# Performance work log

Hardware: AMD Instinct MI355X
Metric: run time of the kernel (lower is better)

Reference implementation:

```python
import jax, jax.numpy as jnp
import numpy as np

N = 1048576          # nodes at current depth (children), divisible by 8
M = N // 8           # non-empty parent nodes (conv outputs)
NNUM_PARENT = 262144 # total parent nodes at depth-1
C_IN = 128
C_OUT = 256


def setup_inputs() -> dict:
    key = jax.random.key(0)
    k1, k2, k3 = jax.random.split(key, 3)
    data = jax.random.normal(k1, (N, C_IN), dtype=jnp.float32)
    weights = jax.random.normal(k2, (8, C_IN, C_OUT), dtype=jnp.float32) * (1.0 / np.sqrt(8 * C_IN))
    # sorted unique positions of non-empty parents within [0, NNUM_PARENT)
    perm = jax.random.permutation(k3, NNUM_PARENT)
    nempty_idx = jnp.sort(perm[:M]).astype(jnp.int32)
    return {"data": data, "weights": weights, "nempty_idx": nempty_idx,
            "nnum_parent": NNUM_PARENT}


def reference(data, weights, nempty_idx, nnum_parent):
    # kernel-2 stride-2 conv: each consecutive group of 8 children -> one parent
    c_in, c_out = weights.shape[1], weights.shape[2]
    out = data.reshape(-1, 8 * c_in) @ weights.reshape(8 * c_in, c_out)  # [M, C_out]
    # octree_pad at depth-1: scatter into all parent nodes, zeros at empty ones
    full = jnp.zeros((nnum_parent, c_out), dtype=out.dtype).at[nempty_idx].set(out)
    return full
```

## Files before the change

### kernel.cpp

```cpp
#include <hip/hip_runtime.h>
#include <hip/hip_bf16.h>

typedef float f32x4 __attribute__((ext_vector_type(4)));
typedef short s16x8 __attribute__((ext_vector_type(8)));

using bf16 = __hip_bfloat16;

namespace {
constexpr int KD = 1024;
constexpr int BM = 128;
constexpr int BK = 32;
constexpr int NT = KD / BK;
constexpr int MBLK = 131072 / BM;
constexpr int ZBLK = 512;
}

typedef __attribute__((address_space(1))) const void GVoid;
typedef __attribute__((address_space(3))) void LVoid;

__device__ __forceinline__ void gld16(const void* g, void* l) {
  __builtin_amdgcn_global_load_lds((GVoid*)g, (LVoid*)l, 16, 0, 0);
}

__device__ __forceinline__ s16x8 cvt8(f32x4 a, f32x4 b) {
  union { s16x8 v; bf16 h[8]; } u;
#pragma unroll
  for (int j = 0; j < 4; ++j) u.h[j] = __float2bfloat16(a[j]);
#pragma unroll
  for (int j = 0; j < 4; ++j) u.h[j + 4] = __float2bfloat16(b[j]);
  return u.v;
}

__global__ void k_transpose_w(const float* __restrict__ w, bf16* __restrict__ bt) {
  int t = blockIdx.x * 256 + threadIdx.x;
  int n = t & 255;
  int k0 = (t >> 8) << 3;
  union { s16x8 v; bf16 h[8]; } u;
#pragma unroll
  for (int j = 0; j < 8; ++j)
    u.h[j] = __float2bfloat16(w[(size_t)(k0 + j) * 256 + n]);
  *(s16x8*)(bt + (size_t)n * KD + k0) = u.v;
}

__global__ void k_clear_flags(int* __restrict__ flags, int np4) {
  int i = blockIdx.x * 256 + threadIdx.x;
  if (i < np4) ((int4*)flags)[i] = make_int4(0, 0, 0, 0);
}

__global__ void k_set_flags(const int* __restrict__ idx, int* __restrict__ flags, int m) {
  int i = blockIdx.x * 256 + threadIdx.x;
  if (i < m) flags[idx[i]] = 1;
}

__global__ __launch_bounds__(512, 4)
void k_fused(const float* __restrict__ A, const bf16* __restrict__ Bt,
             const int* __restrict__ idx, const int* __restrict__ flags,
             float* __restrict__ out, int NP) {
  __shared__ float As[4][BM * BK];

  const int tid = threadIdx.x;
  const int lane = tid & 63;
  const int wave = tid >> 6;
  const int bid = blockIdx.x;

  if (bid % 3 == 2) {
    const int zb = bid / 3;
    const f32x4 z = {0.f, 0.f, 0.f, 0.f};
    for (int row = zb * 8 + wave; row < NP; row += ZBLK * 8) {
      if (flags[row] == 0)
        *(f32x4*)(out + (size_t)row * 256 + lane * 4) = z;
    }
    return;
  }

  const int gid = (bid / 3) * 2 + (bid % 3);
  const int m0 = gid * BM;
  const int wm = wave >> 2;
  const int wn = wave & 3;

  const int as0 = tid, as1 = 512 + tid;
  const int ar0 = as0 >> 3, ac0 = (as0 & 7) ^ (ar0 & 6);
  const int ar1 = as1 >> 3, ac1 = (as1 & 7) ^ (ar1 & 6);
  const float* aSrc0 = A + (size_t)(m0 + ar0) * KD + ac0 * 4;
  const float* aSrc1 = A + (size_t)(m0 + ar1) * KD + ac1 * 4;
  const int aOff0 = (wave * 64) * 4;
  const int aOff1 = (512 + wave * 64) * 4;

  const int r = lane & 15;
  const int kc = lane >> 4;

  const int arow = wm * 64 + r;
  const int aRd = arow * 32 + (((2 * kc) ^ (arow & 6)) * 4);

  const bf16* bp0 = Bt + (size_t)(wn * 64 + r) * KD + kc * 8;
  const bf16* bp1 = bp0 + (size_t)16 * KD;
  const bf16* bp2 = bp0 + (size_t)32 * KD;
  const bf16* bp3 = bp0 + (size_t)48 * KD;

  f32x4 acc[4][4] = {};

  auto stage = [&](int buf, int t) {
    gld16(aSrc0 + t * BK, &As[buf][aOff0]);
    gld16(aSrc1 + t * BK, &As[buf][aOff1]);
  };

  stage(0, 0);
  stage(1, 1);
  stage(2, 2);

#pragma unroll 1
  for (int t = 0; t < NT; ++t) {
    if (t >= 2 && t < NT - 2) {
      asm volatile("s_waitcnt vmcnt(12)" ::: "memory");
    } else if (t == 1) {
      asm volatile("s_waitcnt vmcnt(8)" ::: "memory");
    } else {
      asm volatile("s_waitcnt vmcnt(4)" ::: "memory");
    }
    __builtin_amdgcn_s_barrier();

    s16x8 bfr0 = *(const s16x8*)(bp0 + t * BK);
    s16x8 bfr1 = *(const s16x8*)(bp1 + t * BK);
    s16x8 bfr2 = *(const s16x8*)(bp2 + t * BK);
    s16x8 bfr3 = *(const s16x8*)(bp3 + t * BK);
    asm volatile("" ::: "memory");

    if (t + 3 < NT) stage((t + 3) & 3, t + 3);

    const int cur = t & 3;
#pragma unroll
    for (int fm = 0; fm < 4; ++fm) {
      f32x4 lo = *(const f32x4*)(&As[cur][aRd + fm * 512]);
      f32x4 hi = *(const f32x4*)(&As[cur][aRd + fm * 512 + 4]);
      s16x8 af = cvt8(lo, hi);
      acc[fm][0] = __builtin_amdgcn_mfma_f32_16x16x32_bf16(af, bfr0, acc[fm][0], 0, 0, 0);
      acc[fm][1] = __builtin_amdgcn_mfma_f32_16x16x32_bf16(af, bfr1, acc[fm][1], 0, 0, 0);
      acc[fm][2] = __builtin_amdgcn_mfma_f32_16x16x32_bf16(af, bfr2, acc[fm][2], 0, 0, 0);
      acc[fm][3] = __builtin_amdgcn_mfma_f32_16x16x32_bf16(af, bfr3, acc[fm][3], 0, 0, 0);
    }
  }

  const int col0 = wn * 64 + r;
  const int rb = m0 + wm * 64 + (kc << 2);
#pragma unroll
  for (int fm = 0; fm < 4; ++fm) {
    const int4 rows = *(const int4*)(idx + rb + fm * 16);
    const int rj[4] = {rows.x, rows.y, rows.z, rows.w};
#pragma unroll
    for (int j = 0; j < 4; ++j) {
      float* op = out + (size_t)rj[j] * 256 + col0;
#pragma unroll
      for (int fn = 0; fn < 4; ++fn)
        op[fn * 16] = acc[fm][fn][j];
    }
  }
}

extern "C" void kernel_launch(void* const* d_in, const int* in_sizes, int n_in,
                              void* d_out, int out_size, void* d_ws, size_t ws_size,
                              hipStream_t stream) {
  const float* data = (const float*)d_in[0];
  const float* w    = (const float*)d_in[1];
  const int*   idx  = (const int*)d_in[2];
  float* out = (float*)d_out;

  const int M  = in_sizes[2];
  const int NP = out_size / 256;

  int* flags = (int*)d_ws;
  bf16* bt = (bf16*)((char*)d_ws + (size_t)NP * sizeof(int));

  k_transpose_w<<<128, 256, 0, stream>>>(w, bt);
  k_clear_flags<<<(NP / 4 + 255) / 256, 256, 0, stream>>>(flags, NP / 4);
  k_set_flags<<<(M + 255) / 256, 256, 0, stream>>>(idx, flags, M);
  k_fused<<<MBLK + ZBLK, 512, 0, stream>>>(data, bt, idx, flags, out, NP);
}
```

Baseline: 290.4 us.

## Stage A through registers, convert to bf16 once, double-buffer bf16 LDS

```diff
diff --git a/kernel.cpp b/kernel.cpp
--- a/kernel.cpp
+++ b/kernel.cpp
@@ -13,13 +13,6 @@
 constexpr int NT = KD / BK;
 constexpr int MBLK = 131072 / BM;
 constexpr int ZBLK = 512;
-}
-
-typedef __attribute__((address_space(1))) const void GVoid;
-typedef __attribute__((address_space(3))) void LVoid;
-
-__device__ __forceinline__ void gld16(const void* g, void* l) {
-  __builtin_amdgcn_global_load_lds((GVoid*)g, (LVoid*)l, 16, 0, 0);
 }
 
 __device__ __forceinline__ s16x8 cvt8(f32x4 a, f32x4 b) {
@@ -56,7 +49,7 @@
 void k_fused(const float* __restrict__ A, const bf16* __restrict__ Bt,
              const int* __restrict__ idx, const int* __restrict__ flags,
              float* __restrict__ out, int NP) {
-  __shared__ float As[4][BM * BK];
+  __shared__ bf16 As[2][BM * BK];
 
   const int tid = threadIdx.x;
   const int lane = tid & 63;
@@ -78,66 +71,66 @@
   const int wm = wave >> 2;
   const int wn = wave & 3;
 
-  const int as0 = tid, as1 = 512 + tid;
-  const int ar0 = as0 >> 3, ac0 = (as0 & 7) ^ (ar0 & 6);
-  const int ar1 = as1 >> 3, ac1 = (as1 & 7) ^ (ar1 & 6);
-  const float* aSrc0 = A + (size_t)(m0 + ar0) * KD + ac0 * 4;
-  const float* aSrc1 = A + (size_t)(m0 + ar1) * KD + ac1 * 4;
-  const int aOff0 = (wave * 64) * 4;
-  const int aOff1 = (512 + wave * 64) * 4;
+  const int srow = tid >> 2;
+  const int sc = tid & 3;
+  const float* aSrc = A + (size_t)(m0 + srow) * KD + sc * 8;
+  const int sSlot = srow * 4 + (sc ^ ((srow >> 1) & 3));
 
   const int r = lane & 15;
   const int kc = lane >> 4;
+  const int arow = wm * 64 + r;
+  const int aRd = (arow * 4 + (kc ^ ((arow >> 1) & 3))) * 8;
 
-  const int arow = wm * 64 + r;
-  const int aRd = arow * 32 + (((2 * kc) ^ (arow & 6)) * 4);
-
-  const bf16* bp0 = Bt + (size_t)(wn * 64 + r) * KD + kc * 8;
-  const bf16* bp1 = bp0 + (size_t)16 * KD;
-  const bf16* bp2 = bp0 + (size_t)32 * KD;
-  const bf16* bp3 = bp0 + (size_t)48 * KD;
+  const bf16* bp = Bt + (size_t)(wn * 64 + r) * KD + kc * 8;
 
   f32x4 acc[4][4] = {};
 
-  auto stage = [&](int buf, int t) {
-    gld16(aSrc0 + t * BK, &As[buf][aOff0]);
-    gld16(aSrc1 + t * BK, &As[buf][aOff1]);
+  f32x4 x0, x1, y0, y1;
+  {
+    f32x4 p0 = *(const f32x4*)(aSrc);
+    f32x4 p1 = *(const f32x4*)(aSrc + 4);
+    x0 = *(const f32x4*)(aSrc + BK);
+    x1 = *(const f32x4*)(aSrc + BK + 4);
+    *(s16x8*)(&As[0][sSlot * 8]) = cvt8(p0, p1);
+    asm volatile("s_waitcnt lgkmcnt(0)" ::: "memory");
+    __builtin_amdgcn_sched_barrier(0);
+    __builtin_amdgcn_s_barrier();
+  }
+
+  auto step = [&](int t, f32x4& c0, f32x4& c1, f32x4& n0, f32x4& n1) {
+    s16x8 bv0 = *(const s16x8*)(bp + t * BK);
+    s16x8 bv1 = *(const s16x8*)(bp + (size_t)16 * KD + t * BK);
+    s16x8 bv2 = *(const s16x8*)(bp + (size_t)32 * KD + t * BK);
+    s16x8 bv3 = *(const s16x8*)(bp + (size_t)48 * KD + t * BK);
+    __builtin_amdgcn_sched_barrier(0);
+    if (t + 2 < NT) {
+      n0 = *(const f32x4*)(aSrc + (t + 2) * BK);
+      n1 = *(const f32x4*)(aSrc + (t + 2) * BK + 4);
+    }
+    __builtin_amdgcn_sched_barrier(0);
+
+    const int cur = t & 1;
+#pragma unroll
+    for (int fm = 0; fm < 4; ++fm) {
+      s16x8 af = *(const s16x8*)(&As[cur][aRd + fm * 512]);
+      acc[fm][0] = __builtin_amdgcn_mfma_f32_16x16x32_bf16(af, bv0, acc[fm][0], 0, 0, 0);
+      acc[fm][1] = __builtin_amdgcn_mfma_f32_16x16x32_bf16(af, bv1, acc[fm][1], 0, 0, 0);
+      acc[fm][2] = __builtin_amdgcn_mfma_f32_16x16x32_bf16(af, bv2, acc[fm][2], 0, 0, 0);
+      acc[fm][3] = __builtin_amdgcn_mfma_f32_16x16x32_bf16(af, bv3, acc[fm][3], 0, 0, 0);
+    }
+    __builtin_amdgcn_sched_barrier(0);
+
+    if (t + 1 < NT)
+      *(s16x8*)(&As[cur ^ 1][sSlot * 8]) = cvt8(c0, c1);
+    asm volatile("s_waitcnt lgkmcnt(0)" ::: "memory");
+    __builtin_amdgcn_sched_barrier(0);
+    __builtin_amdgcn_s_barrier();
   };
 
-  stage(0, 0);
-  stage(1, 1);
-  stage(2, 2);
-
 #pragma unroll 1
-  for (int t = 0; t < NT; ++t) {
-    if (t >= 2 && t < NT - 2) {
-      asm volatile("s_waitcnt vmcnt(12)" ::: "memory");
-    } else if (t == 1) {
-      asm volatile("s_waitcnt vmcnt(8)" ::: "memory");
-    } else {
-      asm volatile("s_waitcnt vmcnt(4)" ::: "memory");
-    }
-    __builtin_amdgcn_s_barrier();
-
-    s16x8 bfr0 = *(const s16x8*)(bp0 + t * BK);
-    s16x8 bfr1 = *(const s16x8*)(bp1 + t * BK);
-    s16x8 bfr2 = *(const s16x8*)(bp2 + t * BK);
-    s16x8 bfr3 = *(const s16x8*)(bp3 + t * BK);
-    asm volatile("" ::: "memory");
-
-    if (t + 3 < NT) stage((t + 3) & 3, t + 3);
-
-    const int cur = t & 3;
-#pragma unroll
-    for (int fm = 0; fm < 4; ++fm) {
-      f32x4 lo = *(const f32x4*)(&As[cur][aRd + fm * 512]);
-      f32x4 hi = *(const f32x4*)(&As[cur][aRd + fm * 512 + 4]);
-      s16x8 af = cvt8(lo, hi);
-      acc[fm][0] = __builtin_amdgcn_mfma_f32_16x16x32_bf16(af, bfr0, acc[fm][0], 0, 0, 0);
-      acc[fm][1] = __builtin_amdgcn_mfma_f32_16x16x32_bf16(af, bfr1, acc[fm][1], 0, 0, 0);
-      acc[fm][2] = __builtin_amdgcn_mfma_f32_16x16x32_bf16(af, bfr2, acc[fm][2], 0, 0, 0);
-      acc[fm][3] = __builtin_amdgcn_mfma_f32_16x16x32_bf16(af, bfr3, acc[fm][3], 0, 0, 0);
-    }
+  for (int t = 0; t < NT; t += 2) {
+    step(t,     x0, x1, y0, y1);
+    step(t + 1, y0, y1, x0, x1);
   }
 
   const int col0 = wn * 64 + r;
```

Result: slower. 298.2 us (+2.7%).
